# Performance work log

Hardware: AMD Instinct MI355X
Metric: run time of the kernel (lower is better)

The kernel has to match this reference:

```python
import jax, jax.numpy as jnp
import numpy as np

INPUT_SIZE = 1024
HIDDEN_SIZE = 1024
BATCH = 8192


def setup_inputs() -> dict:
    key = jax.random.key(0)
    ks = jax.random.split(key, 10)
    s_in = 1.0 / np.sqrt(INPUT_SIZE)
    s_h = 1.0 / np.sqrt(HIDDEN_SIZE)
    return {
        "input": jax.random.normal(ks[0], (BATCH, INPUT_SIZE), jnp.float32),
        "hx": jax.random.normal(ks[1], (BATCH, HIDDEN_SIZE), jnp.float32),
        # weights stored [in, out] (transpose of torch Linear)
        "W_ih": jax.random.uniform(ks[2], (INPUT_SIZE, 2 * HIDDEN_SIZE), jnp.float32, -s_in, s_in),
        "b_ih": jax.random.uniform(ks[3], (2 * HIDDEN_SIZE,), jnp.float32, -s_in, s_in),
        "W_hh": jax.random.uniform(ks[4], (HIDDEN_SIZE, 2 * HIDDEN_SIZE), jnp.float32, -s_h, s_h),
        "b_hh": jax.random.uniform(ks[5], (2 * HIDDEN_SIZE,), jnp.float32, -s_h, s_h),
        "W_c": jax.random.uniform(ks[6], (INPUT_SIZE, HIDDEN_SIZE), jnp.float32, -s_in, s_in),
        "b_c": jax.random.uniform(ks[7], (HIDDEN_SIZE,), jnp.float32, -s_in, s_in),
        "W_hc": jax.random.uniform(ks[8], (HIDDEN_SIZE, HIDDEN_SIZE), jnp.float32, -s_h, s_h),
        "b_hc": jax.random.uniform(ks[9], (HIDDEN_SIZE,), jnp.float32, -s_h, s_h),
    }


def reference(input, hx, W_ih, b_ih, W_hh, b_hh, W_c, b_c, W_hc, b_hc):
    H = hx.shape[1]
    gates = jax.nn.sigmoid(input @ W_ih + b_ih + hx @ W_hh + b_hh)  # [B, 2H]
    z_t, r_t = gates[:, :H], gates[:, H:]
    candidate = jnp.tanh(input @ W_c + b_c + r_t * (hx @ W_hc + b_hc))
    return (1.0 - z_t) * hx + z_t * candidate
```

## Files before the change

kernel.cpp:

```cpp
#include <hip/hip_runtime.h>
#include <hip/hip_bf16.h>
#include <cmath>


typedef __attribute__((ext_vector_type(8))) short bf16x8;
typedef __attribute__((ext_vector_type(4))) float f32x4;
typedef unsigned int u32;

typedef const __attribute__((address_space(1))) u32 gu32;
typedef __attribute__((address_space(3))) u32 su32;

__device__ __forceinline__ unsigned short f2bf(float f) {
  union { float f; u32 u; } v; v.f = f;
  u32 u = v.u;
  u += 0x7FFFu + ((u >> 16) & 1u);
  return (unsigned short)(u >> 16);
}

__device__ __forceinline__ void gload16(void* ldsp, const void* gp) {
  __builtin_amdgcn_global_load_lds((gu32*)gp, (su32*)ldsp, 16, 0, 0);
}

__device__ __forceinline__ float sigmf(float x) { return 1.0f / (1.0f + __expf(-x)); }

__global__ __launch_bounds__(256) void cvt_all(
    const float* __restrict__ In, const float* __restrict__ Hx,
    const float* __restrict__ Wih, const float* __restrict__ Whh,
    const float* __restrict__ Wc,  const float* __restrict__ Whc,
    unsigned short* __restrict__ wsIn, unsigned short* __restrict__ wsHx,
    unsigned short* __restrict__ wsWih, unsigned short* __restrict__ wsWhh,
    unsigned short* __restrict__ wsWc,  unsigned short* __restrict__ wsWhc)
{
  int bid = blockIdx.x;
  if (bid < 8192) {
    int gid = bid * 256 + threadIdx.x;
    const float* src; unsigned short* dst; int idx;
    if (gid < (1 << 20)) { src = In; dst = wsIn; idx = gid; }
    else                 { src = Hx; dst = wsHx; idx = gid - (1 << 20); }
    int m = idx >> 7;
    int t = idx & 127;
    const float4* s = (const float4*)(src + (size_t)m * 1024 + t * 8);
    float4 a = s[0], b = s[1];
    int row = m & 127;
    size_t tile = (size_t)(m >> 7) * 32 + (t >> 2);
    int sw = (t & 3) ^ ((row >> 1) & 3);
    bf16x8 v;
    v[0] = (short)f2bf(a.x); v[1] = (short)f2bf(a.y); v[2] = (short)f2bf(a.z); v[3] = (short)f2bf(a.w);
    v[4] = (short)f2bf(b.x); v[5] = (short)f2bf(b.y); v[6] = (short)f2bf(b.z); v[7] = (short)f2bf(b.w);
    *(bf16x8*)(dst + tile * 4096 + row * 32 + sw * 8) = v;
  } else {
    int wb = bid - 8192;
    const float* W; unsigned short* dst; int NW; int local;
    if (wb < 1024)      { W = Wih; dst = wsWih; NW = 2048; local = wb; }
    else if (wb < 2048) { W = Whh; dst = wsWhh; NW = 2048; local = wb - 1024; }
    else if (wb < 2560) { W = Wc;  dst = wsWc;  NW = 1024; local = wb - 2048; }
    else                { W = Whc; dst = wsWhc; NW = 1024; local = wb - 2560; }
    int nb = local >> 5, kb = local & 31;
    int n  = nb * 64 + (threadIdx.x & 63);
    int k0 = kb * 32 + (threadIdx.x >> 6) * 8;
    unsigned short h[8];
    #pragma unroll
    for (int b = 0; b < 8; ++b) h[b] = f2bf(W[(size_t)(k0 + b) * NW + n]);
    int row = n & 63;
    size_t tile = (size_t)(n >> 6) * 32 + (k0 >> 5);
    int sw = ((k0 >> 3) & 3) ^ ((row >> 1) & 3);
    bf16x8 v;
    #pragma unroll
    for (int b = 0; b < 8; ++b) v[b] = (short)h[b];
    *(bf16x8*)(dst + tile * 2048 + row * 32 + sw * 8) = v;
  }
}

__global__ __launch_bounds__(256, 2) void gru_gemm(
    const unsigned short* __restrict__ wsIn, const unsigned short* __restrict__ wsHx,
    const unsigned short* __restrict__ wsWih, const unsigned short* __restrict__ wsWhh,
    const unsigned short* __restrict__ wsWc, const unsigned short* __restrict__ wsWhc,
    const float* __restrict__ Hx,
    const float* __restrict__ bih, const float* __restrict__ bhh,
    const float* __restrict__ bc, const float* __restrict__ bhc,
    float* __restrict__ out)
{
  __shared__ unsigned short lds[40960];
  const int tid  = threadIdx.x;
  const int lane = tid & 63;
  const int wave = tid >> 6;
  const int wm = wave >> 1, wn = wave & 1;
  const int bid = blockIdx.x;
  const int j = bid & 15;
  const int i = bid >> 4;

  const unsigned short* srcB[10];
  int strd[10];
  #pragma unroll
  for (int c0 = 0; c0 < 10; ++c0) {
    int c = wave * 10 + c0;
    const unsigned short* p; int st;
    if (c < 8)       { p = wsIn + (size_t)i * 131072 + c * 512;        st = 4096; }
    else if (c < 16) { p = wsHx + (size_t)i * 131072 + (c - 8) * 512;  st = 4096; }
    else {
      int t = (c - 16) >> 2, cc = (c - 16) & 3;
      const unsigned short* base; int nb;
      if (t == 0)      { base = wsWih; nb = j; }
      else if (t == 1) { base = wsWih; nb = j + 16; }
      else if (t == 2) { base = wsWhh; nb = j; }
      else if (t == 3) { base = wsWhh; nb = j + 16; }
      else if (t == 4) { base = wsWc;  nb = j; }
      else             { base = wsWhc; nb = j; }
      p = base + (size_t)nb * 65536 + cc * 512;
      st = 2048;
    }
    srcB[c0] = p + lane * 8;
    strd[c0] = st;
  }
  const int stageOff = (wave * 10) * 512;

  f32x4 accZ[4][2], accR[4][2], accC[4][2], accH[4][2];
  #pragma unroll
  for (int a = 0; a < 4; ++a)
    #pragma unroll
    for (int b = 0; b < 2; ++b) {
      accZ[a][b] = (f32x4)(0.0f); accR[a][b] = (f32x4)(0.0f);
      accC[a][b] = (f32x4)(0.0f); accH[a][b] = (f32x4)(0.0f);
    }

  const int r15 = lane & 15;
  const int q   = lane >> 4;

  int aOff[4], wOff[2];
  #pragma unroll
  for (int mr = 0; mr < 4; ++mr) {
    int row = wm * 64 + mr * 16 + r15;
    aOff[mr] = row * 32 + ((q ^ ((row >> 1) & 3)) << 3);
  }
  #pragma unroll
  for (int nr = 0; nr < 2; ++nr) {
    int row = wn * 32 + nr * 16 + r15;
    wOff[nr] = row * 32 + ((q ^ ((row >> 1) & 3)) << 3);
  }

  auto stage = [&](int bufBase, int s) {
    #pragma unroll
    for (int c0 = 0; c0 < 10; ++c0)
      gload16((void*)&lds[bufBase + stageOff + c0 * 512],
              (const void*)(srcB[c0] + (size_t)s * strd[c0]));
  };

  auto compute = [&](const unsigned short* __restrict__ L) {
    bf16x8 aIn[4], aHx[4];
    #pragma unroll
    for (int mr = 0; mr < 4; ++mr) {
      aIn[mr] = *(const bf16x8*)&L[aOff[mr]];
      aHx[mr] = *(const bf16x8*)&L[4096 + aOff[mr]];
    }
    bf16x8 wf[6][2];
    #pragma unroll
    for (int t = 0; t < 6; ++t)
      #pragma unroll
      for (int nr = 0; nr < 2; ++nr)
        wf[t][nr] = *(const bf16x8*)&L[8192 + t * 2048 + wOff[nr]];

    __builtin_amdgcn_s_setprio(1);
    #pragma unroll
    for (int mr = 0; mr < 4; ++mr)
      #pragma unroll
      for (int nr = 0; nr < 2; ++nr) {
        accZ[mr][nr] = __builtin_amdgcn_mfma_f32_16x16x32_bf16(aIn[mr], wf[0][nr], accZ[mr][nr], 0, 0, 0);
        accZ[mr][nr] = __builtin_amdgcn_mfma_f32_16x16x32_bf16(aHx[mr], wf[2][nr], accZ[mr][nr], 0, 0, 0);
        accR[mr][nr] = __builtin_amdgcn_mfma_f32_16x16x32_bf16(aIn[mr], wf[1][nr], accR[mr][nr], 0, 0, 0);
        accR[mr][nr] = __builtin_amdgcn_mfma_f32_16x16x32_bf16(aHx[mr], wf[3][nr], accR[mr][nr], 0, 0, 0);
        accC[mr][nr] = __builtin_amdgcn_mfma_f32_16x16x32_bf16(aIn[mr], wf[4][nr], accC[mr][nr], 0, 0, 0);
        accH[mr][nr] = __builtin_amdgcn_mfma_f32_16x16x32_bf16(aHx[mr], wf[5][nr], accH[mr][nr], 0, 0, 0);
      }
    __builtin_amdgcn_s_setprio(0);
  };

  stage(0, 0);
  __syncthreads();

  #pragma unroll 1
  for (int it = 0; it < 16; ++it) {
    const int s = it * 2;
    stage(20480, s + 1);
    __builtin_amdgcn_sched_barrier(0);
    compute(&lds[0]);
    __syncthreads();
    if (it < 15) stage(0, s + 2);
    __builtin_amdgcn_sched_barrier(0);
    compute(&lds[20480]);
    __syncthreads();
  }

  const int n0 = j * 64 + wn * 32;
  const int m0 = i * 128 + wm * 64;
  #pragma unroll
  for (int nr = 0; nr < 2; ++nr) {
    int n = n0 + nr * 16 + r15;
    float bz  = bih[n] + bhh[n];
    float br  = bih[1024 + n] + bhh[1024 + n];
    float bcv = bc[n], bhcv = bhc[n];
    #pragma unroll
    for (int mr = 0; mr < 4; ++mr) {
      #pragma unroll
      for (int v = 0; v < 4; ++v) {
        int m = m0 + mr * 16 + q * 4 + v;
        float z  = sigmf(accZ[mr][nr][v] + bz);
        float rr = sigmf(accR[mr][nr][v] + br);
        float cd = tanhf(accC[mr][nr][v] + bcv + rr * (accH[mr][nr][v] + bhcv));
        float h  = Hx[(size_t)m * 1024 + n];
        out[(size_t)m * 1024 + n] = (1.0f - z) * h + z * cd;
      }
    }
  }
}

__global__ __launch_bounds__(256) void gru_fallback(
    const float* __restrict__ In, const float* __restrict__ Hx,
    const float* __restrict__ Wih, const float* __restrict__ bih,
    const float* __restrict__ Whh, const float* __restrict__ bhh,
    const float* __restrict__ Wc, const float* __restrict__ bc,
    const float* __restrict__ Whc, const float* __restrict__ bhc,
    float* __restrict__ out)
{
  __shared__ float sIn[64][17], sHx[64][17];
  __shared__ float sW[6][16][68];
  const int tid = threadIdx.x;
  const int j = blockIdx.x & 15, i = blockIdx.x >> 4;
  const int tx = tid & 15, ty = tid >> 4;
  float accZ[4][4] = {}, accR[4][4] = {}, accC[4][4] = {}, accH[4][4] = {};
  const int ms = tid >> 2, kq = (tid & 3) * 4;
  const int wk = tid >> 4, wn4 = (tid & 15) * 4;
  for (int k0 = 0; k0 < 1024; k0 += 16) {
    __syncthreads();
    {
      float4 a = *(const float4*)&In[(size_t)(i * 64 + ms) * 1024 + k0 + kq];
      sIn[ms][kq] = a.x; sIn[ms][kq + 1] = a.y; sIn[ms][kq + 2] = a.z; sIn[ms][kq + 3] = a.w;
      float4 b = *(const float4*)&Hx[(size_t)(i * 64 + ms) * 1024 + k0 + kq];
      sHx[ms][kq] = b.x; sHx[ms][kq + 1] = b.y; sHx[ms][kq + 2] = b.z; sHx[ms][kq + 3] = b.w;
    }
    {
      float4 w0 = *(const float4*)&Wih[(size_t)(k0 + wk) * 2048 + j * 64 + wn4];
      float4 w1 = *(const float4*)&Wih[(size_t)(k0 + wk) * 2048 + 1024 + j * 64 + wn4];
      float4 w2 = *(const float4*)&Whh[(size_t)(k0 + wk) * 2048 + j * 64 + wn4];
      float4 w3 = *(const float4*)&Whh[(size_t)(k0 + wk) * 2048 + 1024 + j * 64 + wn4];
      float4 w4 = *(const float4*)&Wc[(size_t)(k0 + wk) * 1024 + j * 64 + wn4];
      float4 w5 = *(const float4*)&Whc[(size_t)(k0 + wk) * 1024 + j * 64 + wn4];
      sW[0][wk][wn4] = w0.x; sW[0][wk][wn4+1] = w0.y; sW[0][wk][wn4+2] = w0.z; sW[0][wk][wn4+3] = w0.w;
      sW[1][wk][wn4] = w1.x; sW[1][wk][wn4+1] = w1.y; sW[1][wk][wn4+2] = w1.z; sW[1][wk][wn4+3] = w1.w;
      sW[2][wk][wn4] = w2.x; sW[2][wk][wn4+1] = w2.y; sW[2][wk][wn4+2] = w2.z; sW[2][wk][wn4+3] = w2.w;
      sW[3][wk][wn4] = w3.x; sW[3][wk][wn4+1] = w3.y; sW[3][wk][wn4+2] = w3.z; sW[3][wk][wn4+3] = w3.w;
      sW[4][wk][wn4] = w4.x; sW[4][wk][wn4+1] = w4.y; sW[4][wk][wn4+2] = w4.z; sW[4][wk][wn4+3] = w4.w;
      sW[5][wk][wn4] = w5.x; sW[5][wk][wn4+1] = w5.y; sW[5][wk][wn4+2] = w5.z; sW[5][wk][wn4+3] = w5.w;
    }
    __syncthreads();
    for (int kk = 0; kk < 16; ++kk) {
      float aI[4], aH[4];
      #pragma unroll
      for (int im = 0; im < 4; ++im) { aI[im] = sIn[ty * 4 + im][kk]; aH[im] = sHx[ty * 4 + im][kk]; }
      #pragma unroll
      for (int jn = 0; jn < 4; ++jn) {
        float w0 = sW[0][kk][tx * 4 + jn], w1 = sW[1][kk][tx * 4 + jn], w2 = sW[2][kk][tx * 4 + jn];
        float w3 = sW[3][kk][tx * 4 + jn], w4 = sW[4][kk][tx * 4 + jn], w5 = sW[5][kk][tx * 4 + jn];
        #pragma unroll
        for (int im = 0; im < 4; ++im) {
          accZ[im][jn] += aI[im] * w0 + aH[im] * w2;
          accR[im][jn] += aI[im] * w1 + aH[im] * w3;
          accC[im][jn] += aI[im] * w4;
          accH[im][jn] += aH[im] * w5;
        }
      }
    }
  }
  #pragma unroll
  for (int jn = 0; jn < 4; ++jn) {
    int n = j * 64 + tx * 4 + jn;
    float bz  = bih[n] + bhh[n];
    float br  = bih[1024 + n] + bhh[1024 + n];
    float bcv = bc[n], bhcv = bhc[n];
    #pragma unroll
    for (int im = 0; im < 4; ++im) {
      int m = i * 64 + ty * 4 + im;
      float z  = sigmf(accZ[im][jn] + bz);
      float rr = sigmf(accR[im][jn] + br);
      float cd = tanhf(accC[im][jn] + bcv + rr * (accH[im][jn] + bhcv));
      float h  = Hx[(size_t)m * 1024 + n];
      out[(size_t)m * 1024 + n] = (1.0f - z) * h + z * cd;
    }
  }
}

extern "C" void kernel_launch(void* const* d_in, const int* in_sizes, int n_in,
                              void* d_out, int out_size, void* d_ws, size_t ws_size,
                              hipStream_t stream) {
  const float* In  = (const float*)d_in[0];
  const float* Hx  = (const float*)d_in[1];
  const float* Wih = (const float*)d_in[2];
  const float* bih = (const float*)d_in[3];
  const float* Whh = (const float*)d_in[4];
  const float* bhh = (const float*)d_in[5];
  const float* Wc  = (const float*)d_in[6];
  const float* bc  = (const float*)d_in[7];
  const float* Whc = (const float*)d_in[8];
  const float* bhc = (const float*)d_in[9];
  float* out = (float*)d_out;

  const size_t WS_NEED = 46137344ull;
  if (ws_size >= WS_NEED) {
    unsigned short* ws    = (unsigned short*)d_ws;
    unsigned short* wsIn  = ws;
    unsigned short* wsHx  = ws + 8388608;
    unsigned short* wsWih = ws + 16777216;
    unsigned short* wsWhh = ws + 18874368;
    unsigned short* wsWc  = ws + 20971520;
    unsigned short* wsWhc = ws + 22020096;
    cvt_all<<<11264, 256, 0, stream>>>(In, Hx, Wih, Whh, Wc, Whc,
                                       wsIn, wsHx, wsWih, wsWhh, wsWc, wsWhc);
    gru_gemm<<<1024, 256, 0, stream>>>(wsIn, wsHx, wsWih, wsWhh, wsWc, wsWhc,
                                       Hx, bih, bhh, bc, bhc, out);
  } else {
    gru_fallback<<<2048, 256, 0, stream>>>(In, Hx, Wih, bih, Whh, bhh, Wc, bc, Whc, bhc, out);
  }
}
```

Before: 161.0 us.

## Enlarge GEMM block to 256 rows with 8 waves and swizzled block order

The fused GRU GEMM block grows from 128x64 to 256x64 output using 512 threads, so each weight tile loaded into LDS is reused across twice as many rows. Block indices are swizzled so neighbouring blocks share weight column tiles for better L2 reuse. The pipeline is restructured with explicit waitcnt/barrier control and prefetch two stages ahead, and MFMA work is split into three weight-fragment groups to lower register pressure. In exchange it uses more LDS per block, reduces the grid to 512 blocks, and redundantly loads the last stage near the loop end.

```diff
diff --git a/kernel.cpp b/kernel.cpp
--- a/kernel.cpp
+++ b/kernel.cpp
@@ -71,7 +71,7 @@
   }
 }
 
-__global__ __launch_bounds__(256, 2) void gru_gemm(
+__global__ __launch_bounds__(512, 2) void gru_gemm(
     const unsigned short* __restrict__ wsIn, const unsigned short* __restrict__ wsHx,
     const unsigned short* __restrict__ wsWih, const unsigned short* __restrict__ wsWhh,
     const unsigned short* __restrict__ wsWc, const unsigned short* __restrict__ wsWhc,
@@ -80,25 +80,30 @@
     const float* __restrict__ bc, const float* __restrict__ bhc,
     float* __restrict__ out)
 {
-  __shared__ unsigned short lds[40960];
+  __shared__ unsigned short lds[57344];
   const int tid  = threadIdx.x;
   const int lane = tid & 63;
   const int wave = tid >> 6;
   const int wm = wave >> 1, wn = wave & 1;
   const int bid = blockIdx.x;
-  const int j = bid & 15;
-  const int i = bid >> 4;
-
-  const unsigned short* srcB[10];
-  int strd[10];
-  #pragma unroll
-  for (int c0 = 0; c0 < 10; ++c0) {
-    int c = wave * 10 + c0;
+  const int swz = (bid & 7) * 64 + (bid >> 3);
+  const int j = swz & 15;
+  const int i = swz >> 4;
+
+  const unsigned short* srcB[7];
+  int strd[7];
+  #pragma unroll
+  for (int c0 = 0; c0 < 7; ++c0) {
+    int c = wave * 7 + c0;
     const unsigned short* p; int st;
-    if (c < 8)       { p = wsIn + (size_t)i * 131072 + c * 512;        st = 4096; }
-    else if (c < 16) { p = wsHx + (size_t)i * 131072 + (c - 8) * 512;  st = 4096; }
-    else {
-      int t = (c - 16) >> 2, cc = (c - 16) & 3;
+    if (c < 16) {
+      int mt = 2 * i + (c >> 3);
+      p = wsIn + (size_t)mt * 131072 + (c & 7) * 512; st = 4096;
+    } else if (c < 32) {
+      int cc = c - 16; int mt = 2 * i + (cc >> 3);
+      p = wsHx + (size_t)mt * 131072 + (cc & 7) * 512; st = 4096;
+    } else {
+      int t = (c - 32) >> 2, cc = (c - 32) & 3;
       const unsigned short* base; int nb;
       if (t == 0)      { base = wsWih; nb = j; }
       else if (t == 1) { base = wsWih; nb = j + 16; }
@@ -106,13 +111,12 @@
       else if (t == 3) { base = wsWhh; nb = j + 16; }
       else if (t == 4) { base = wsWc;  nb = j; }
       else             { base = wsWhc; nb = j; }
-      p = base + (size_t)nb * 65536 + cc * 512;
-      st = 2048;
+      p = base + (size_t)nb * 65536 + cc * 512; st = 2048;
     }
     srcB[c0] = p + lane * 8;
     strd[c0] = st;
   }
-  const int stageOff = (wave * 10) * 512;
+  const int ldsC = wave * 3584;
 
   f32x4 accZ[4][2], accR[4][2], accC[4][2], accH[4][2];
   #pragma unroll
@@ -129,69 +133,97 @@
   int aOff[4], wOff[2];
   #pragma unroll
   for (int mr = 0; mr < 4; ++mr) {
-    int row = wm * 64 + mr * 16 + r15;
-    aOff[mr] = row * 32 + ((q ^ ((row >> 1) & 3)) << 3);
+    int gr = wm * 64 + mr * 16 + r15;
+    aOff[mr] = (gr >> 7) * 4096 + (gr & 127) * 32 + ((q ^ ((gr >> 1) & 3)) << 3);
   }
   #pragma unroll
   for (int nr = 0; nr < 2; ++nr) {
-    int row = wn * 32 + nr * 16 + r15;
-    wOff[nr] = row * 32 + ((q ^ ((row >> 1) & 3)) << 3);
-  }
-
-  auto stage = [&](int bufBase, int s) {
-    #pragma unroll
-    for (int c0 = 0; c0 < 10; ++c0)
-      gload16((void*)&lds[bufBase + stageOff + c0 * 512],
+    int wr = wn * 32 + nr * 16 + r15;
+    wOff[nr] = 16384 + wr * 32 + ((q ^ ((wr >> 1) & 3)) << 3);
+  }
+
+  auto stage = [&](int B, int s) {
+    #pragma unroll
+    for (int c0 = 0; c0 < 7; ++c0)
+      gload16((void*)&lds[B + ldsC + c0 * 512],
               (const void*)(srcB[c0] + (size_t)s * strd[c0]));
   };
 
-  auto compute = [&](const unsigned short* __restrict__ L) {
+  auto step = [&](int B, int s2) {
     bf16x8 aIn[4], aHx[4];
     #pragma unroll
     for (int mr = 0; mr < 4; ++mr) {
-      aIn[mr] = *(const bf16x8*)&L[aOff[mr]];
-      aHx[mr] = *(const bf16x8*)&L[4096 + aOff[mr]];
-    }
-    bf16x8 wf[6][2];
-    #pragma unroll
-    for (int t = 0; t < 6; ++t)
-      #pragma unroll
-      for (int nr = 0; nr < 2; ++nr)
-        wf[t][nr] = *(const bf16x8*)&L[8192 + t * 2048 + wOff[nr]];
-
+      aIn[mr] = *(const bf16x8*)&lds[B + aOff[mr]];
+      aHx[mr] = *(const bf16x8*)&lds[B + 8192 + aOff[mr]];
+    }
     __builtin_amdgcn_s_setprio(1);
-    #pragma unroll
-    for (int mr = 0; mr < 4; ++mr)
+    {
+      bf16x8 wa[2], wb[2];
       #pragma unroll
       for (int nr = 0; nr < 2; ++nr) {
-        accZ[mr][nr] = __builtin_amdgcn_mfma_f32_16x16x32_bf16(aIn[mr], wf[0][nr], accZ[mr][nr], 0, 0, 0);
-        accZ[mr][nr] = __builtin_amdgcn_mfma_f32_16x16x32_bf16(aHx[mr], wf[2][nr], accZ[mr][nr], 0, 0, 0);
-        accR[mr][nr] = __builtin_amdgcn_mfma_f32_16x16x32_bf16(aIn[mr], wf[1][nr], accR[mr][nr], 0, 0, 0);
-        accR[mr][nr] = __builtin_amdgcn_mfma_f32_16x16x32_bf16(aHx[mr], wf[3][nr], accR[mr][nr], 0, 0, 0);
-        accC[mr][nr] = __builtin_amdgcn_mfma_f32_16x16x32_bf16(aIn[mr], wf[4][nr], accC[mr][nr], 0, 0, 0);
-        accH[mr][nr] = __builtin_amdgcn_mfma_f32_16x16x32_bf16(aHx[mr], wf[5][nr], accH[mr][nr], 0, 0, 0);
-      }
+        wa[nr] = *(const bf16x8*)&lds[B + wOff[nr]];
+        wb[nr] = *(const bf16x8*)&lds[B + 4096 + wOff[nr]];
+      }
+      #pragma unroll
+      for (int mr = 0; mr < 4; ++mr)
+        #pragma unroll
+        for (int nr = 0; nr < 2; ++nr) {
+          accZ[mr][nr] = __builtin_amdgcn_mfma_f32_16x16x32_bf16(aIn[mr], wa[nr], accZ[mr][nr], 0, 0, 0);
+          accZ[mr][nr] = __builtin_amdgcn_mfma_f32_16x16x32_bf16(aHx[mr], wb[nr], accZ[mr][nr], 0, 0, 0);
+        }
+    }
+    {
+      bf16x8 wa[2], wb[2];
+      #pragma unroll
+      for (int nr = 0; nr < 2; ++nr) {
+        wa[nr] = *(const bf16x8*)&lds[B + 2048 + wOff[nr]];
+        wb[nr] = *(const bf16x8*)&lds[B + 6144 + wOff[nr]];
+      }
+      #pragma unroll
+      for (int mr = 0; mr < 4; ++mr)
+        #pragma unroll
+        for (int nr = 0; nr < 2; ++nr) {
+          accR[mr][nr] = __builtin_amdgcn_mfma_f32_16x16x32_bf16(aIn[mr], wa[nr], accR[mr][nr], 0, 0, 0);
+          accR[mr][nr] = __builtin_amdgcn_mfma_f32_16x16x32_bf16(aHx[mr], wb[nr], accR[mr][nr], 0, 0, 0);
+        }
+    }
+    {
+      bf16x8 wa[2], wb[2];
+      #pragma unroll
+      for (int nr = 0; nr < 2; ++nr) {
+        wa[nr] = *(const bf16x8*)&lds[B + 8192 + wOff[nr]];
+        wb[nr] = *(const bf16x8*)&lds[B + 10240 + wOff[nr]];
+      }
+      #pragma unroll
+      for (int mr = 0; mr < 4; ++mr)
+        #pragma unroll
+        for (int nr = 0; nr < 2; ++nr) {
+          accC[mr][nr] = __builtin_amdgcn_mfma_f32_16x16x32_bf16(aIn[mr], wa[nr], accC[mr][nr], 0, 0, 0);
+          accH[mr][nr] = __builtin_amdgcn_mfma_f32_16x16x32_bf16(aHx[mr], wb[nr], accH[mr][nr], 0, 0, 0);
+        }
+    }
     __builtin_amdgcn_s_setprio(0);
+    asm volatile("s_waitcnt lgkmcnt(0)" ::: "memory");
+    __builtin_amdgcn_s_barrier();
+    stage(B, s2);
+    asm volatile("s_waitcnt vmcnt(7)" ::: "memory");
+    __builtin_amdgcn_s_barrier();
   };
 
   stage(0, 0);
-  __syncthreads();
+  stage(28672, 1);
+  asm volatile("s_waitcnt vmcnt(7)" ::: "memory");
+  __builtin_amdgcn_s_barrier();
 
   #pragma unroll 1
   for (int it = 0; it < 16; ++it) {
     const int s = it * 2;
-    stage(20480, s + 1);
-    __builtin_amdgcn_sched_barrier(0);
-    compute(&lds[0]);
-    __syncthreads();
-    if (it < 15) stage(0, s + 2);
-    __builtin_amdgcn_sched_barrier(0);
-    compute(&lds[20480]);
-    __syncthreads();
+    step(0,     s + 2 <= 31 ? s + 2 : 31);
+    step(28672, s + 3 <= 31 ? s + 3 : 31);
   }
 
   const int n0 = j * 64 + wn * 32;
-  const int m0 = i * 128 + wm * 64;
+  const int m0 = i * 256 + wm * 64;
   #pragma unroll
   for (int nr = 0; nr < 2; ++nr) {
     int n = n0 + nr * 16 + r15;
@@ -314,8 +346,8 @@
     unsigned short* wsWhc = ws + 22020096;
     cvt_all<<<11264, 256, 0, stream>>>(In, Hx, Wih, Whh, Wc, Whc,
                                        wsIn, wsHx, wsWih, wsWhh, wsWc, wsWhc);
-    gru_gemm<<<1024, 256, 0, stream>>>(wsIn, wsHx, wsWih, wsWhh, wsWc, wsWhc,
-                                       Hx, bih, bhh, bc, bhc, out);
+    gru_gemm<<<512, 512, 0, stream>>>(wsIn, wsHx, wsWih, wsWhh, wsWc, wsWhc,
+                                      Hx, bih, bhh, bc, bhc, out);
   } else {
     gru_fallback<<<2048, 256, 0, stream>>>(In, Hx, Wih, bih, Whh, bhh, Wc, bc, Whc, bhc, out);
   }
```

Measured after the change: 135.6 us. 1.19x faster.

## Restructure GRU into large-tile 256x256 GEMM with bf16 intermediates and separate epilogue

Applied to the files above, without the earlier changes.

Adds a new path, taken when the workspace is large enough, that converts inputs and weights into 256-row, 64-wide K tiles with an XOR swizzle. A 512-thread GEMM kernel then computes 256x256 output tiles, each block handling one of the Z/R gates plus either the C or H product. Gate sigmoids are applied in-kernel and the pre-activations are written as bf16 to workspace. A third elementwise kernel combines them with hx to form the output. The larger tiles raise data reuse per LDS load, at the cost of extra global traffic for the intermediates, an extra launch, and bf16 rounding of the gate values. The old mid-size path is also simplified to single buffering.

```diff
diff --git a/kernel.cpp b/kernel.cpp
--- a/kernel.cpp
+++ b/kernel.cpp
@@ -16,14 +16,255 @@
   u += 0x7FFFu + ((u >> 16) & 1u);
   return (unsigned short)(u >> 16);
 }
-
+__device__ __forceinline__ float bfu(u32 w) {
+  union { u32 u; float f; } c; c.u = (w & 0xffffu) << 16; return c.f;
+}
 __device__ __forceinline__ void gload16(void* ldsp, const void* gp) {
   __builtin_amdgcn_global_load_lds((gu32*)gp, (su32*)ldsp, 16, 0, 0);
 }
-
 __device__ __forceinline__ float sigmf(float x) { return 1.0f / (1.0f + __expf(-x)); }
 
-__global__ __launch_bounds__(256) void cvt_all(
+__global__ __launch_bounds__(256) void cvt2(
+    const float* __restrict__ In, const float* __restrict__ Hx,
+    const float* __restrict__ Wih, const float* __restrict__ Whh,
+    const float* __restrict__ Wc,  const float* __restrict__ Whc,
+    unsigned short* __restrict__ wsIn, unsigned short* __restrict__ wsHx,
+    unsigned short* __restrict__ wsW)
+{
+  int bid = blockIdx.x;
+  if (bid < 8192) {
+    int gid = bid * 256 + threadIdx.x;
+    const float* src; unsigned short* dst; int idx;
+    if (gid < (1 << 20)) { src = In; dst = wsIn; idx = gid; }
+    else                 { src = Hx; dst = wsHx; idx = gid - (1 << 20); }
+    int m = idx >> 7, u = idx & 127;
+    int kt = u >> 3, s = u & 7;
+    const float4* p = (const float4*)(src + (size_t)m * 1024 + kt * 64 + s * 8);
+    float4 a = p[0], b = p[1];
+    int row = m & 255, mt = m >> 8;
+    int sp = s ^ (row & 7);
+    bf16x8 v;
+    v[0] = (short)f2bf(a.x); v[1] = (short)f2bf(a.y); v[2] = (short)f2bf(a.z); v[3] = (short)f2bf(a.w);
+    v[4] = (short)f2bf(b.x); v[5] = (short)f2bf(b.y); v[6] = (short)f2bf(b.z); v[7] = (short)f2bf(b.w);
+    *(bf16x8*)(dst + (size_t)(mt * 16 + kt) * 16384 + row * 64 + sp * 8) = v;
+  } else {
+    int w = bid - 8192;
+    int j = w / 384, rem = w % 384;
+    int t = rem >> 3, s = rem & 7;
+    int jj = j & 3, f = j >> 2;
+    int row = threadIdx.x;
+    const float* W; int NW, k0, ncol;
+    if (t < 16)      { W = Wih; NW = 2048; k0 = t * 64 + s * 8;        ncol = f * 1024 + jj * 256 + row; }
+    else if (t < 32) { W = Whh; NW = 2048; k0 = (t - 16) * 64 + s * 8; ncol = f * 1024 + jj * 256 + row; }
+    else             { W = f ? Whc : Wc; NW = 1024; k0 = (t - 32) * 64 + s * 8; ncol = jj * 256 + row; }
+    bf16x8 v;
+    #pragma unroll
+    for (int b = 0; b < 8; ++b) v[b] = (short)f2bf(W[(size_t)(k0 + b) * NW + ncol]);
+    int sp = s ^ (row & 7);
+    *(bf16x8*)(wsW + (size_t)(j * 48 + t) * 16384 + row * 64 + sp * 8) = v;
+  }
+}
+
+__global__ __launch_bounds__(512, 2) void gru_gemm1(
+    const unsigned short* __restrict__ wsIn, const unsigned short* __restrict__ wsHx,
+    const unsigned short* __restrict__ wsW,
+    unsigned short* __restrict__ actZ, unsigned short* __restrict__ actR,
+    unsigned short* __restrict__ actC, unsigned short* __restrict__ actH,
+    const float* __restrict__ bih, const float* __restrict__ bhh)
+{
+  __shared__ unsigned short lds[65536];
+  char* LB = (char*)lds;
+  const int tid = threadIdx.x, lane = tid & 63, wave = tid >> 6;
+  const int wm = wave >> 2, wn = wave & 3;
+  const int j = blockIdx.x & 7, i = blockIdx.x >> 3;
+  const int jj = j & 3, f = j >> 2;
+  const int r15 = lane & 15, q = lane >> 4, x7 = r15 & 7;
+
+  int aOff[8][2], bOff[4][2];
+  #pragma unroll
+  for (int mr = 0; mr < 8; ++mr)
+    #pragma unroll
+    for (int kk = 0; kk < 2; ++kk)
+      aOff[mr][kk] = (wm * 128 + mr * 16 + r15) * 128 + (((kk * 4 + q) ^ x7) << 4);
+  #pragma unroll
+  for (int nr = 0; nr < 4; ++nr)
+    #pragma unroll
+    for (int kk = 0; kk < 2; ++kk)
+      bOff[nr][kk] = 65536 + (wn * 64 + nr * 16 + r15) * 128 + (((kk * 4 + q) ^ x7) << 4);
+
+  const unsigned short* srcW  = wsW + (size_t)j * 48 * 16384;
+  const unsigned short* srcA2 = f ? wsHx : wsIn;
+  const int lo8 = lane * 8;
+
+  auto aSrc = [&](int kt) -> const unsigned short* {
+    const unsigned short* base; int t;
+    if (kt < 16)      { base = wsIn;  t = kt; }
+    else if (kt < 32) { base = wsHx;  t = kt - 16; }
+    else              { base = srcA2; t = kt - 32; }
+    return base + (size_t)(i * 16 + t) * 16384;
+  };
+  auto stageA = [&](int PB, int kt) {
+    const unsigned short* s = aSrc(kt);
+    #pragma unroll
+    for (int c = 0; c < 4; ++c)
+      gload16(LB + PB + (wave * 4 + c) * 1024, s + (wave * 4 + c) * 512 + lo8);
+  };
+  auto stageB = [&](int PB, int kt) {
+    const unsigned short* s = srcW + (size_t)kt * 16384;
+    #pragma unroll
+    for (int c = 0; c < 4; ++c)
+      gload16(LB + 65536 + PB + (wave * 4 + c) * 1024, s + (wave * 4 + c) * 512 + lo8);
+  };
+
+  f32x4 acc[8][4];
+  #pragma unroll
+  for (int mr = 0; mr < 8; ++mr)
+    #pragma unroll
+    for (int nr = 0; nr < 4; ++nr) acc[mr][nr] = (f32x4)(0.0f);
+
+  #define MG(AF, BF, MRB, NRB)                                                      \
+    __builtin_amdgcn_s_setprio(1);                                                  \
+    _Pragma("unroll")                                                               \
+    for (int mr_ = 0; mr_ < 4; ++mr_)                                               \
+      _Pragma("unroll")                                                             \
+      for (int nr_ = 0; nr_ < 2; ++nr_)                                             \
+        _Pragma("unroll")                                                           \
+        for (int kk_ = 0; kk_ < 2; ++kk_)                                           \
+          acc[(MRB)+mr_][(NRB)+nr_] = __builtin_amdgcn_mfma_f32_16x16x32_bf16(      \
+              AF[mr_][kk_], BF[nr_][kk_], acc[(MRB)+mr_][(NRB)+nr_], 0, 0, 0);      \
+    __builtin_amdgcn_s_setprio(0);
+
+  #define TILE(PB, KT, KTN)                                                         \
+  {                                                                                 \
+    bf16x8 a0[4][2], a1[4][2], b0[2][2], b1[2][2];                                  \
+    _Pragma("unroll")                                                               \
+    for (int mr_ = 0; mr_ < 4; ++mr_)                                               \
+      _Pragma("unroll")                                                             \
+      for (int kk_ = 0; kk_ < 2; ++kk_)                                             \
+        a0[mr_][kk_] = *(const bf16x8*)(LB + (PB) + aOff[mr_][kk_]);                \
+    _Pragma("unroll")                                                               \
+    for (int nr_ = 0; nr_ < 2; ++nr_)                                               \
+      _Pragma("unroll")                                                             \
+      for (int kk_ = 0; kk_ < 2; ++kk_)                                             \
+        b0[nr_][kk_] = *(const bf16x8*)(LB + (PB) + bOff[nr_][kk_]);                \
+    MG(a0, b0, 0, 0)                                                                \
+    _Pragma("unroll")                                                               \
+    for (int nr_ = 0; nr_ < 2; ++nr_)                                               \
+      _Pragma("unroll")                                                             \
+      for (int kk_ = 0; kk_ < 2; ++kk_)                                             \
+        b1[nr_][kk_] = *(const bf16x8*)(LB + (PB) + bOff[nr_ + 2][kk_]);            \
+    MG(a0, b1, 0, 2)                                                                \
+    _Pragma("unroll")                                                               \
+    for (int mr_ = 0; mr_ < 4; ++mr_)                                               \
+      _Pragma("unroll")                                                             \
+      for (int kk_ = 0; kk_ < 2; ++kk_)                                             \
+        a1[mr_][kk_] = *(const bf16x8*)(LB + (PB) + aOff[mr_ + 4][kk_]);            \
+    MG(a1, b0, 4, 0)                                                                \
+    asm volatile("s_waitcnt lgkmcnt(0)" ::: "memory");                              \
+    __builtin_amdgcn_sched_barrier(0);                                              \
+    __builtin_amdgcn_s_barrier();                                                   \
+    __builtin_amdgcn_sched_barrier(0);                                              \
+    stageA(PB, KTN);                                                                \
+    MG(a1, b1, 4, 2)                                                                \
+    stageB(PB, KTN);                                                                \
+    asm volatile("s_waitcnt vmcnt(8)" ::: "memory");                                \
+    __builtin_amdgcn_sched_barrier(0);                                              \
+    __builtin_amdgcn_s_barrier();                                                   \
+    __builtin_amdgcn_sched_barrier(0);                                              \
+  }
+
+  auto dump = [&](unsigned short* dst, bool gate, float* bg) {
+    #pragma unroll
+    for (int mr = 0; mr < 8; ++mr)
+      #pragma unroll
+      for (int nr = 0; nr < 4; ++nr) {
+        f32x4 t = acc[mr][nr];
+        float e0, e1, e2, e3;
+        if (gate) {
+          e0 = sigmf(t[0] + bg[nr]); e1 = sigmf(t[1] + bg[nr]);
+          e2 = sigmf(t[2] + bg[nr]); e3 = sigmf(t[3] + bg[nr]);
+        } else { e0 = t[0]; e1 = t[1]; e2 = t[2]; e3 = t[3]; }
+        u32 lo = (u32)f2bf(e0) | ((u32)f2bf(e1) << 16);
+        u32 hi = (u32)f2bf(e2) | ((u32)f2bf(e3) << 16);
+        size_t F = ((size_t)(((i * 2 + wm) * 8 + mr) * 64 + jj * 16 + wn * 4 + nr)) * 256 + lane * 4;
+        uint2 uv; uv.x = lo; uv.y = hi;
+        *(uint2*)(dst + F) = uv;
+        acc[mr][nr] = (f32x4)(0.0f);
+      }
+  };
+
+  stageA(0, 0);     stageB(0, 0);
+  stageA(32768, 1); stageB(32768, 1);
+  asm volatile("s_waitcnt vmcnt(0)" ::: "memory");
+  __builtin_amdgcn_s_barrier();
+  __builtin_amdgcn_sched_barrier(0);
+
+  #pragma unroll 1
+  for (int it = 0; it < 16; ++it) {
+    int kt = 2 * it;
+    TILE(0,     kt,     kt + 2)
+    TILE(32768, kt + 1, kt + 3)
+  }
+
+  {
+    float bg[4];
+    #pragma unroll
+    for (int nr = 0; nr < 4; ++nr) {
+      int gn = jj * 256 + wn * 64 + nr * 16 + r15;
+      int np = f ? 1024 + gn : gn;
+      bg[nr] = bih[np] + bhh[np];
+    }
+    dump(f ? actR : actZ, true, bg);
+  }
+
+  #pragma unroll 1
+  for (int it = 0; it < 8; ++it) {
+    int kt = 32 + 2 * it;
+    int n0 = kt + 2 <= 47 ? kt + 2 : 47;
+    int n1 = kt + 3 <= 47 ? kt + 3 : 47;
+    TILE(0,     kt,     n0)
+    TILE(32768, kt + 1, n1)
+  }
+
+  dump(f ? actH : actC, false, nullptr);
+  #undef TILE
+  #undef MG
+}
+
+__global__ __launch_bounds__(256) void gru_final(
+    const unsigned short* __restrict__ actZ, const unsigned short* __restrict__ actR,
+    const unsigned short* __restrict__ actC, const unsigned short* __restrict__ actH,
+    const float* __restrict__ Hx, const float* __restrict__ bc,
+    const float* __restrict__ bhc, float* __restrict__ out)
+{
+  int T = blockIdx.x * 256 + threadIdx.x;
+  int lane = T & 63, fr = T >> 6;
+  int nr = fr & 3, wn = (fr >> 2) & 3, jj = (fr >> 4) & 3, mr = (fr >> 6) & 7, wmI = fr >> 9;
+  int n  = jj * 256 + wn * 64 + nr * 16 + (lane & 15);
+  int m0 = wmI * 128 + mr * 16 + ((lane >> 4) << 2);
+  size_t off = (size_t)T * 4;
+  uint2 zq = *(const uint2*)(actZ + off);
+  uint2 rq = *(const uint2*)(actR + off);
+  uint2 cq = *(const uint2*)(actC + off);
+  uint2 hq = *(const uint2*)(actH + off);
+  float bcv = bc[n], bhv = bhc[n];
+  u32 zw[2] = { zq.x, zq.y }, rw[2] = { rq.x, rq.y };
+  u32 cw[2] = { cq.x, cq.y }, hw[2] = { hq.x, hq.y };
+  #pragma unroll
+  for (int v = 0; v < 4; ++v) {
+    int sh = (v & 1) * 16, ix = v >> 1;
+    float z = bfu(zw[ix] >> sh);
+    float r = bfu(rw[ix] >> sh);
+    float c = bfu(cw[ix] >> sh);
+    float h = bfu(hw[ix] >> sh);
+    size_t adr = (size_t)(m0 + v) * 1024 + n;
+    float hx = Hx[adr];
+    float cand = tanhf(c + bcv + r * (h + bhv));
+    out[adr] = (1.0f - z) * hx + z * cand;
+  }
+}
+
+__global__ __launch_bounds__(256) void cvt_m(
     const float* __restrict__ In, const float* __restrict__ Hx,
     const float* __restrict__ Wih, const float* __restrict__ Whh,
     const float* __restrict__ Wc,  const float* __restrict__ Whc,
@@ -37,8 +278,7 @@
     const float* src; unsigned short* dst; int idx;
     if (gid < (1 << 20)) { src = In; dst = wsIn; idx = gid; }
     else                 { src = Hx; dst = wsHx; idx = gid - (1 << 20); }
-    int m = idx >> 7;
-    int t = idx & 127;
+    int m = idx >> 7, t = idx & 127;
     const float4* s = (const float4*)(src + (size_t)m * 1024 + t * 8);
     float4 a = s[0], b = s[1];
     int row = m & 127;
@@ -58,20 +298,17 @@
     int nb = local >> 5, kb = local & 31;
     int n  = nb * 64 + (threadIdx.x & 63);
     int k0 = kb * 32 + (threadIdx.x >> 6) * 8;
-    unsigned short h[8];
-    #pragma unroll
-    for (int b = 0; b < 8; ++b) h[b] = f2bf(W[(size_t)(k0 + b) * NW + n]);
+    bf16x8 v;
+    #pragma unroll
+    for (int b = 0; b < 8; ++b) v[b] = (short)f2bf(W[(size_t)(k0 + b) * NW + n]);
     int row = n & 63;
     size_t tile = (size_t)(n >> 6) * 32 + (k0 >> 5);
     int sw = ((k0 >> 3) & 3) ^ ((row >> 1) & 3);
-    bf16x8 v;
-    #pragma unroll
-    for (int b = 0; b < 8; ++b) v[b] = (short)h[b];
     *(bf16x8*)(dst + tile * 2048 + row * 32 + sw * 8) = v;
   }
 }
 
-__global__ __launch_bounds__(256, 2) void gru_gemm(
+__global__ __launch_bounds__(256, 2) void gemm_m(
     const unsigned short* __restrict__ wsIn, const unsigned short* __restrict__ wsHx,
     const unsigned short* __restrict__ wsWih, const unsigned short* __restrict__ wsWhh,
     const unsigned short* __restrict__ wsWc, const unsigned short* __restrict__ wsWhc,
@@ -80,7 +317,7 @@
     const float* __restrict__ bc, const float* __restrict__ bhc,
     float* __restrict__ out)
 {
-  __shared__ unsigned short lds[40960];
+  __shared__ unsigned short lds[20480];
   const int tid  = threadIdx.x;
   const int lane = tid & 63;
   const int wave = tid >> 6;
@@ -88,7 +325,6 @@
   const int bid = blockIdx.x;
   const int j = bid & 15;
   const int i = bid >> 4;
-
   const unsigned short* srcB[10];
   int strd[10];
   #pragma unroll
@@ -112,8 +348,6 @@
     srcB[c0] = p + lane * 8;
     strd[c0] = st;
   }
-  const int stageOff = (wave * 10) * 512;
-
   f32x4 accZ[4][2], accR[4][2], accC[4][2], accH[4][2];
   #pragma unroll
   for (int a = 0; a < 4; ++a)
@@ -122,10 +356,8 @@
       accZ[a][b] = (f32x4)(0.0f); accR[a][b] = (f32x4)(0.0f);
       accC[a][b] = (f32x4)(0.0f); accH[a][b] = (f32x4)(0.0f);
     }
-
   const int r15 = lane & 15;
   const int q   = lane >> 4;
-
   int aOff[4], wOff[2];
   #pragma unroll
   for (int mr = 0; mr < 4; ++mr) {
@@ -137,29 +369,25 @@
     int row = wn * 32 + nr * 16 + r15;
     wOff[nr] = row * 32 + ((q ^ ((row >> 1) & 3)) << 3);
   }
-
-  auto stage = [&](int bufBase, int s) {
+  for (int s = 0; s < 32; ++s) {
+    __syncthreads();
     #pragma unroll
     for (int c0 = 0; c0 < 10; ++c0)
-      gload16((void*)&lds[bufBase + stageOff + c0 * 512],
+      gload16((void*)&lds[(wave * 10 + c0) * 512],
               (const void*)(srcB[c0] + (size_t)s * strd[c0]));
-  };
-
-  auto compute = [&](const unsigned short* __restrict__ L) {
+    __syncthreads();
     bf16x8 aIn[4], aHx[4];
     #pragma unroll
     for (int mr = 0; mr < 4; ++mr) {
-      aIn[mr] = *(const bf16x8*)&L[aOff[mr]];
-      aHx[mr] = *(const bf16x8*)&L[4096 + aOff[mr]];
+      aIn[mr] = *(const bf16x8*)&lds[aOff[mr]];
+      aHx[mr] = *(const bf16x8*)&lds[4096 + aOff[mr]];
     }
     bf16x8 wf[6][2];
     #pragma unroll
     for (int t = 0; t < 6; ++t)
       #pragma unroll
       for (int nr = 0; nr < 2; ++nr)
-        wf[t][nr] = *(const bf16x8*)&L[8192 + t * 2048 + wOff[nr]];
-
-    __builtin_amdgcn_s_setprio(1);
+        wf[t][nr] = *(const bf16x8*)&lds[8192 + t * 2048 + wOff[nr]];
     #pragma unroll
     for (int mr = 0; mr < 4; ++mr)
       #pragma unroll
@@ -171,25 +399,7 @@
         accC[mr][nr] = __builtin_amdgcn_mfma_f32_16x16x32_bf16(aIn[mr], wf[4][nr], accC[mr][nr], 0, 0, 0);
         accH[mr][nr] = __builtin_amdgcn_mfma_f32_16x16x32_bf16(aHx[mr], wf[5][nr], accH[mr][nr], 0, 0, 0);
       }
-    __builtin_amdgcn_s_setprio(0);
-  };
-
-  stage(0, 0);
-  __syncthreads();
-
-  #pragma unroll 1
-  for (int it = 0; it < 16; ++it) {
-    const int s = it * 2;
-    stage(20480, s + 1);
-    __builtin_amdgcn_sched_barrier(0);
-    compute(&lds[0]);
-    __syncthreads();
-    if (it < 15) stage(0, s + 2);
-    __builtin_amdgcn_sched_barrier(0);
-    compute(&lds[20480]);
-    __syncthreads();
-  }
-
+  }
   const int n0 = j * 64 + wn * 32;
   const int m0 = i * 128 + wm * 64;
   #pragma unroll
@@ -303,8 +513,21 @@
   const float* bhc = (const float*)d_in[9];
   float* out = (float*)d_out;
 
-  const size_t WS_NEED = 46137344ull;
-  if (ws_size >= WS_NEED) {
+  const size_t WS_BIG = 113246208ull;
+  const size_t WS_MID = 46137344ull;
+  if (ws_size >= WS_BIG) {
+    unsigned short* ws   = (unsigned short*)d_ws;
+    unsigned short* wsIn = ws;
+    unsigned short* wsHx = ws + 8388608;
+    unsigned short* wsW  = ws + 16777216;
+    unsigned short* actZ = ws + 23068672;
+    unsigned short* actR = ws + 31457280;
+    unsigned short* actC = ws + 39845888;
+    unsigned short* actH = ws + 48234496;
+    cvt2<<<11264, 256, 0, stream>>>(In, Hx, Wih, Whh, Wc, Whc, wsIn, wsHx, wsW);
+    gru_gemm1<<<256, 512, 0, stream>>>(wsIn, wsHx, wsW, actZ, actR, actC, actH, bih, bhh);
+    gru_final<<<8192, 256, 0, stream>>>(actZ, actR, actC, actH, Hx, bc, bhc, out);
+  } else if (ws_size >= WS_MID) {
     unsigned short* ws    = (unsigned short*)d_ws;
     unsigned short* wsIn  = ws;
     unsigned short* wsHx  = ws + 8388608;
@@ -312,10 +535,10 @@
     unsigned short* wsWhh = ws + 18874368;
     unsigned short* wsWc  = ws + 20971520;
     unsigned short* wsWhc = ws + 22020096;
-    cvt_all<<<11264, 256, 0, stream>>>(In, Hx, Wih, Whh, Wc, Whc,
-                                       wsIn, wsHx, wsWih, wsWhh, wsWc, wsWhc);
-    gru_gemm<<<1024, 256, 0, stream>>>(wsIn, wsHx, wsWih, wsWhh, wsWc, wsWhc,
-                                       Hx, bih, bhh, bc, bhc, out);
+    cvt_m<<<11264, 256, 0, stream>>>(In, Hx, Wih, Whh, Wc, Whc,
+                                     wsIn, wsHx, wsWih, wsWhh, wsWc, wsWhc);
+    gemm_m<<<1024, 256, 0, stream>>>(wsIn, wsHx, wsWih, wsWhh, wsWc, wsWhc,
+                                     Hx, bih, bhh, bc, bhc, out);
   } else {
     gru_fallback<<<2048, 256, 0, stream>>>(In, Hx, Wih, bih, Whh, bhh, Wc, bc, Whc, bhc, out);
   }
```

Result: faster. 156.3 us (-2.9%).
